# Kernel optimization log

Hardware: AMD Instinct MI355X
Metric: run time of the kernel (lower is better)

## Reference

```python
import jax, jax.numpy as jnp
import numpy as np

REGION_DIM = 144
LLM_DIM = 3584
NUM_HEADS = 4
HEAD_DIM = REGION_DIM // NUM_HEADS          # 36
V_HEAD_DIM = LLM_DIM // NUM_HEADS           # 896
LN_EPS = 1e-5
N, M = 4096, 4096


def setup_inputs() -> dict:
    key = jax.random.key(0)
    ks = jax.random.split(key, 16)
    s = 0.02
    return {
        "target_emb": jax.random.normal(ks[0], (N, REGION_DIM), jnp.float32),
        "source_emb": jax.random.normal(ks[1], (M, LLM_DIM), jnp.float32),
        "value_emb":  jax.random.normal(ks[2], (M, LLM_DIM), jnp.float32),
        # params stored [in, out] (transposed vs torch nn.Linear)
        "wq_w": jax.random.normal(ks[3], (REGION_DIM, REGION_DIM), jnp.float32) * s,
        "wq_b": jnp.zeros((REGION_DIM,), jnp.float32),
        "wk_w": jax.random.normal(ks[4], (LLM_DIM, REGION_DIM), jnp.float32) * s,
        "wk_b": jnp.zeros((REGION_DIM,), jnp.float32),
        # per-head V projections stacked: [H, llm_dim, llm_dim//H]
        "wv_w": jax.random.normal(ks[5], (NUM_HEADS, LLM_DIM, V_HEAD_DIM), jnp.float32) * s,
        "wv_b": jnp.zeros((NUM_HEADS, V_HEAD_DIM), jnp.float32),
        "resid_w": jax.random.normal(ks[6], (REGION_DIM, LLM_DIM), jnp.float32) * s,
        "resid_b": jnp.zeros((LLM_DIM,), jnp.float32),
        "out_w": jax.random.normal(ks[7], (LLM_DIM, LLM_DIM), jnp.float32) * s,
        "out_b": jnp.zeros((LLM_DIM,), jnp.float32),
        "ln_g": jnp.ones((LLM_DIM,), jnp.float32),
        "ln_b": jnp.zeros((LLM_DIM,), jnp.float32),
    }


def reference(target_emb, source_emb, value_emb,
              wq_w, wq_b, wk_w, wk_b, wv_w, wv_b,
              resid_w, resid_b, out_w, out_b, ln_g, ln_b):
    n = target_emb.shape[0]
    # Q: [N, region_dim] -> [H, N, head_dim]; K: [M, llm_dim] -> [H, M, head_dim]
    Q = (target_emb @ wq_w + wq_b).reshape(n, NUM_HEADS, HEAD_DIM).transpose(1, 0, 2)
    K = (source_emb @ wk_w + wk_b).reshape(-1, NUM_HEADS, HEAD_DIM).transpose(1, 0, 2)
    scores = jnp.einsum('hnd,hmd->hnm', Q, K) / jnp.sqrt(jnp.float32(HEAD_DIM))
    attn = jax.nn.softmax(scores, axis=-1)      # dropout = identity (eval mode)
    # per-head value projections: [H, M, llm_dim//H]
    V = jnp.einsum('me,hed->hmd', value_emb, wv_w) + wv_b[:, None, :]
    ctx = jnp.einsum('hnm,hmd->nhd', attn, V).reshape(n, LLM_DIM)
    x = ctx + (target_emb @ resid_w + resid_b)   # residual_proj (region_dim != llm_dim)
    mu = jnp.mean(x, axis=-1, keepdims=True)
    var = jnp.mean(jnp.square(x - mu), axis=-1, keepdims=True)
    x = (x - mu) * jax.lax.rsqrt(var + LN_EPS) * ln_g + ln_b
    return x @ out_w + out_b
```

## Files before the change

### kernel.cpp

```cpp
#include <hip/hip_runtime.h>

typedef _Float16 f16;
typedef _Float16 f16x8 __attribute__((ext_vector_type(8)));
typedef float f32x4 __attribute__((ext_vector_type(4)));

#define REGION_DIM 144
#define LLM_DIM 3584
#define NUM_HEADS 4
#define HEAD_DIM 36
#define HEAD_PAD 64
#define QK_COLS 256
#define KPAD_REGION 160
#define V_HEAD 896
#define LN_EPS 1e-5f

__device__ __forceinline__ void gl_lds16(const f16* g, f16* l)
{
    __builtin_amdgcn_global_load_lds(
        (const __attribute__((address_space(1))) unsigned int*)g,
        (__attribute__((address_space(3))) unsigned int*)l, 16, 0, 0);
}

#define S_BARRIER() do { asm volatile("" ::: "memory"); __builtin_amdgcn_s_barrier(); asm volatile("" ::: "memory"); } while (0)
#define WAIT_LGKM0() asm volatile("s_waitcnt lgkmcnt(0)" ::: "memory")
#define SCHED_FENCE() __builtin_amdgcn_sched_barrier(0)

__global__ void k_convert_pad(const float* __restrict__ in, f16* __restrict__ out,
                              int Cin, int Cout)
{
    int r = blockIdx.y;
    int c = blockIdx.x * 256 + threadIdx.x;
    if (c >= Cout) return;
    float v = (c < Cin) ? in[(long)r * Cin + c] : 0.f;
    out[(long)r * Cout + c] = (f16)v;
}

__global__ void k_transpose(const float* __restrict__ in, f16* __restrict__ out,
                            int R, int C, int Rpad, int Cpad,
                            long in_bstride, long out_bstride)
{
    __shared__ float tile[32][33];
    const float* ip = in + (long)blockIdx.z * in_bstride;
    f16* op = out + (long)blockIdx.z * out_bstride;
    int r0 = blockIdx.y * 32, c0 = blockIdx.x * 32;
    int tx = threadIdx.x, ty = threadIdx.y;
#pragma unroll
    for (int i = 0; i < 32; i += 8) {
        int r = r0 + ty + i, c = c0 + tx;
        tile[ty + i][tx] = (r < R && c < C) ? ip[(long)r * C + c] : 0.f;
    }
    __syncthreads();
#pragma unroll
    for (int i = 0; i < 32; i += 8) {
        int c = c0 + ty + i, r = r0 + tx;
        if (c < Cpad && r < Rpad) op[(long)c * Rpad + r] = (f16)tile[tx][ty + i];
    }
}

__global__ void k_headpad_w(const float* __restrict__ w, const float* __restrict__ b,
                            f16* __restrict__ outW, float* __restrict__ outB,
                            int E, int Epad)
{
    int hp = blockIdx.y;
    int h = hp >> 6, kk = hp & 63;
    int d = h * HEAD_DIM + kk;
    bool valid = (kk < HEAD_DIM);
    int e = blockIdx.x * 256 + threadIdx.x;
    if (e < Epad) {
        float v = (valid && e < E) ? w[(long)e * REGION_DIM + d] : 0.f;
        outW[(long)hp * Epad + e] = (f16)v;
    }
    if (blockIdx.x == 0 && threadIdx.x == 0) outB[hp] = valid ? b[d] : 0.f;
}

enum { EPI_F16_EXPSCALE = 0,
       EPI_F16_BIASROW  = 1,
       EPI_F16_DIVROW   = 2,
       EPI_F32_BIASCOL  = 3,
       EPI_F16_BIASCOL  = 4 };

template <int EPI>
__global__ __launch_bounds__(256, 2)
void gemm_f16(const f16* __restrict__ A, int lda, long sAz,
              const f16* __restrict__ Bt, int ldb, long sBz,
              void* __restrict__ Cv, int ldc, long sCz,
              const float* __restrict__ bias, long sbz, float scale, int K)
{
    __shared__ __align__(16) f16 sA[128 * 32];
    __shared__ __align__(16) f16 sB[128 * 32];
    const int tid = threadIdx.x;
    const int z = blockIdx.z;
    A += (long)z * sAz;
    Bt += (long)z * sBz;
    if (bias) bias += (long)z * sbz;

    const int gx = gridDim.x, gy = gridDim.y;
    int pid = blockIdx.y * gx + blockIdx.x;
    const int GROUP = 8;
    int span = GROUP * gx;
    int gid = pid / span;
    int y0 = gid * GROUP;
    int gsz = (gy - y0 < GROUP) ? (gy - y0) : GROUP;
    int rem = pid - gid * span;
    const int by = y0 + rem % gsz;
    const int bx = rem / gsz;
    const int m0 = by * 128, n0 = bx * 128;

    const int w = tid >> 6, l = tid & 63;
    const int wu = __builtin_amdgcn_readfirstlane(w);
    const int wr = w >> 1, wc = w & 1;

    f32x4 acc[4][4] = {};

    const int srow = tid >> 2;
    const int scol = (tid & 3) * 8;
    const f16* Ag = A + (long)(m0 + srow) * lda + scol;
    const f16* Bg = Bt + (long)(n0 + srow) * ldb + scol;
    f16* sA0 = sA + wu * 512;
    f16* sA1 = sA + 2048 + wu * 512;
    f16* sB0 = sB + wu * 512;
    f16* sB1 = sB + 2048 + wu * 512;
    const int qk = (l >> 4) * 8;
    const int fr = l & 15;

    for (int k0 = 0; k0 < K; k0 += 32) {
        __syncthreads();
        gl_lds16(Ag + k0, sA0);
        gl_lds16(Ag + (long)64 * lda + k0, sA1);
        gl_lds16(Bg + k0, sB0);
        gl_lds16(Bg + (long)64 * ldb + k0, sB1);
        __syncthreads();

        f16x8 af[4], bf[4];
#pragma unroll
        for (int mt = 0; mt < 4; mt++)
            af[mt] = *(const f16x8*)&sA[(wr * 64 + mt * 16 + fr) * 32 + qk];
#pragma unroll
        for (int nt = 0; nt < 4; nt++)
            bf[nt] = *(const f16x8*)&sB[(wc * 64 + nt * 16 + fr) * 32 + qk];
#pragma unroll
        for (int mt = 0; mt < 4; mt++)
#pragma unroll
            for (int nt = 0; nt < 4; nt++)
                acc[mt][nt] = __builtin_amdgcn_mfma_f32_16x16x32_f16(af[mt], bf[nt], acc[mt][nt], 0, 0, 0);
    }

    const int q4 = (l >> 4) * 4;
    float bc[4];
#pragma unroll
    for (int nt = 0; nt < 4; nt++) {
        if constexpr (EPI == EPI_F16_BIASCOL || EPI == EPI_F32_BIASCOL)
            bc[nt] = bias[n0 + wc * 64 + nt * 16 + fr];
        else
            bc[nt] = 0.f;
    }
#pragma unroll
    for (int mt = 0; mt < 4; mt++)
#pragma unroll
        for (int r = 0; r < 4; r++) {
            int row = m0 + wr * 64 + mt * 16 + q4 + r;
            float rowv = 0.f;
            if constexpr (EPI == EPI_F16_BIASROW) rowv = bias[row];
            if constexpr (EPI == EPI_F16_DIVROW) rowv = 1.f / bias[row];
#pragma unroll
            for (int nt = 0; nt < 4; nt++) {
                int col = n0 + wc * 64 + nt * 16 + fr;
                float v = acc[mt][nt][r];
                if constexpr (EPI == EPI_F16_EXPSCALE) {
                    ((f16*)Cv + (long)z * sCz)[(long)row * ldc + col] = (f16)__expf(v * scale);
                } else if constexpr (EPI == EPI_F16_BIASROW) {
                    ((f16*)Cv + (long)z * sCz)[(long)row * ldc + col] = (f16)(v + rowv);
                } else if constexpr (EPI == EPI_F16_DIVROW) {
                    ((f16*)Cv + (long)z * sCz)[(long)row * ldc + col] = (f16)(v * rowv);
                } else if constexpr (EPI == EPI_F16_BIASCOL) {
                    ((f16*)Cv + (long)z * sCz)[(long)row * ldc + col] = (f16)(v + bc[nt]);
                } else {
                    ((float*)Cv + (long)z * sCz)[(long)row * ldc + col] = v + bc[nt];
                }
            }
        }
}

template <int EPI>
__global__ __launch_bounds__(512, 2)
void gemm256_f16(const f16* __restrict__ A, int lda,
                 const f16* __restrict__ Bt, int ldb,
                 void* __restrict__ Cv, int ldc,
                 const float* __restrict__ bias, int K)
{
    __shared__ __align__(16) f16 sm[65536];
    f16* smf = sm;

    const int tid = threadIdx.x;
    const int l = tid & 63;

    const int gx = gridDim.x, gy = gridDim.y;
    int pid = blockIdx.y * gx + blockIdx.x;
    int nwg = gx * gy;
    int q = nwg >> 3, r8 = nwg & 7;
    int xcd = pid & 7, idx = pid >> 3;
    int swz = (xcd < r8) ? (xcd * (q + 1) + idx)
                         : (r8 * (q + 1) + (xcd - r8) * q + idx);
    const int by = swz % gy, bx = swz / gy;
    const int m0 = by * 256, n0 = bx * 256;

    const int wu = __builtin_amdgcn_readfirstlane(tid >> 6);
    const int wr = wu >> 2;
    const int wc = wu & 3;
    const int wst = wu * 512;

    const int strow = wu * 8 + (l >> 3);
    const int stcol = ((l & 7) ^ (l >> 3)) * 8;
    const f16* Asrc = A + (size_t)(m0 + strow) * lda + stcol;
    const f16* Bsrc = Bt + (size_t)(n0 + strow) * ldb + stcol;

    const int fr = l & 15;
    const int hi8 = (l >> 4) * 8;
    const int swl = (fr & 7) * 8;
    const int ca0 = hi8 ^ swl;
    const int ca1 = (32 + hi8) ^ swl;

    const int NT = K >> 6;

    f32x4 acc[8][4] = {};
    f16x8 af[4][2], bf0[2][2], bf1[2][2];

    gl_lds16(Asrc, smf + wst);
    gl_lds16(Asrc + (size_t)64 * lda, smf + 4096 + wst);
    gl_lds16(Bsrc, smf + 16384 + wst);
    gl_lds16(Bsrc + (size_t)64 * ldb, smf + 16384 + 4096 + wst);
    gl_lds16(Asrc + (size_t)128 * lda, smf + 8192 + wst);
    gl_lds16(Asrc + (size_t)192 * lda, smf + 8192 + 4096 + wst);
    gl_lds16(Bsrc + (size_t)128 * ldb, smf + 16384 + 8192 + wst);
    gl_lds16(Bsrc + (size_t)192 * ldb, smf + 16384 + 8192 + 4096 + wst);
    if (NT > 1) {
        gl_lds16(Bsrc + 64, smf + 32768 + 16384 + wst);
        gl_lds16(Bsrc + 64 + (size_t)64 * ldb, smf + 32768 + 16384 + 4096 + wst);
        gl_lds16(Asrc + 64, smf + 32768 + wst);
        gl_lds16(Asrc + 64 + (size_t)64 * lda, smf + 32768 + 4096 + wst);
        asm volatile("s_waitcnt vmcnt(4)" ::: "memory");
    } else {
        asm volatile("s_waitcnt vmcnt(0)" ::: "memory");
    }
    S_BARRIER();

#define MFMA16(MB, NB, BF)                                                            \
    _Pragma("unroll") for (int i = 0; i < 4; i++)                                     \
    _Pragma("unroll") for (int j = 0; j < 2; j++) {                                   \
        acc[MB + i][NB + j] = __builtin_amdgcn_mfma_f32_16x16x32_f16(                 \
            af[i][0], BF[j][0], acc[MB + i][NB + j], 0, 0, 0);                        \
        acc[MB + i][NB + j] = __builtin_amdgcn_mfma_f32_16x16x32_f16(                 \
            af[i][1], BF[j][1], acc[MB + i][NB + j], 0, 0, 0);                        \
    }

    for (int t = 0; t < NT; ++t) {
        const int p = t & 1;
        const f16* sAp = smf + (p << 15) + wr * 8192 + fr * 64;
        const f16* sBp = smf + (p << 15) + 16384 + wc * 4096 + fr * 64;

#pragma unroll
        for (int i = 0; i < 4; i++) {
            af[i][0] = *(const f16x8*)(sAp + i * 1024 + ca0);
            af[i][1] = *(const f16x8*)(sAp + i * 1024 + ca1);
        }
#pragma unroll
        for (int j = 0; j < 2; j++) {
            bf0[j][0] = *(const f16x8*)(sBp + j * 1024 + ca0);
            bf0[j][1] = *(const f16x8*)(sBp + j * 1024 + ca1);
        }
        if (t + 1 < NT) {
            const f16* s = Asrc + (size_t)128 * lda + (size_t)(t + 1) * 64;
            f16* d = smf + ((p ^ 1) << 15) + 8192 + wst;
            gl_lds16(s, d);
            gl_lds16(s + (size_t)64 * lda, d + 4096);
        }
        S_BARRIER();
        WAIT_LGKM0();
        SCHED_FENCE();
        __builtin_amdgcn_s_setprio(1);
        MFMA16(0, 0, bf0);
        __builtin_amdgcn_s_setprio(0);
        WAIT_LGKM0();
        S_BARRIER();

#pragma unroll
        for (int j = 0; j < 2; j++) {
            bf1[j][0] = *(const f16x8*)(sBp + 2048 + j * 1024 + ca0);
            bf1[j][1] = *(const f16x8*)(sBp + 2048 + j * 1024 + ca1);
        }
        if (t + 1 < NT) {
            const f16* s = Bsrc + (size_t)128 * ldb + (size_t)(t + 1) * 64;
            f16* d = smf + ((p ^ 1) << 15) + 16384 + 8192 + wst;
            gl_lds16(s, d);
            gl_lds16(s + (size_t)64 * ldb, d + 4096);
        }
        S_BARRIER();
        WAIT_LGKM0();
        SCHED_FENCE();
        __builtin_amdgcn_s_setprio(1);
        MFMA16(0, 2, bf1);
        __builtin_amdgcn_s_setprio(0);
        WAIT_LGKM0();
        S_BARRIER();

#pragma unroll
        for (int i = 0; i < 4; i++) {
            af[i][0] = *(const f16x8*)(sAp + 4096 + i * 1024 + ca0);
            af[i][1] = *(const f16x8*)(sAp + 4096 + i * 1024 + ca1);
        }
        if (t + 2 < NT) {
            const f16* s = Bsrc + (size_t)(t + 2) * 64;
            f16* d = smf + (p << 15) + 16384 + wst;
            gl_lds16(s, d);
            gl_lds16(s + (size_t)64 * ldb, d + 4096);
        }
        S_BARRIER();
        WAIT_LGKM0();
        SCHED_FENCE();
        __builtin_amdgcn_s_setprio(1);
        MFMA16(4, 2, bf1);
        __builtin_amdgcn_s_setprio(0);
        WAIT_LGKM0();
        S_BARRIER();

        if (t + 2 < NT) {
            const f16* s = Asrc + (size_t)(t + 2) * 64;
            f16* d = smf + (p << 15) + wst;
            gl_lds16(s, d);
            gl_lds16(s + (size_t)64 * lda, d + 4096);
        }
        S_BARRIER();
        __builtin_amdgcn_s_setprio(1);
        MFMA16(4, 0, bf0);
        __builtin_amdgcn_s_setprio(0);
        if (t + 2 < NT) {
            asm volatile("s_waitcnt vmcnt(4)" ::: "memory");
        } else if (t + 1 < NT) {
            asm volatile("s_waitcnt vmcnt(0)" ::: "memory");
        }
        S_BARRIER();
    }
#undef MFMA16

    const int q4 = (l >> 4) * 4;
    float bc[4];
#pragma unroll
    for (int nt = 0; nt < 4; nt++) {
        if constexpr (EPI == EPI_F16_BIASCOL || EPI == EPI_F32_BIASCOL)
            bc[nt] = bias[n0 + wc * 64 + nt * 16 + fr];
        else
            bc[nt] = 0.f;
    }
#pragma unroll
    for (int mt = 0; mt < 8; mt++)
#pragma unroll
        for (int r = 0; r < 4; r++) {
            int row = m0 + wr * 128 + mt * 16 + q4 + r;
            float rowv = 0.f;
            if constexpr (EPI == EPI_F16_BIASROW) rowv = bias[row];
            if constexpr (EPI == EPI_F16_DIVROW) rowv = 1.f / bias[row];
#pragma unroll
            for (int nt = 0; nt < 4; nt++) {
                int col = n0 + wc * 64 + nt * 16 + fr;
                float v = acc[mt][nt][r];
                if constexpr (EPI == EPI_F16_BIASROW) {
                    ((f16*)Cv)[(size_t)row * ldc + col] = (f16)(v + rowv);
                } else if constexpr (EPI == EPI_F16_DIVROW) {
                    ((f16*)Cv)[(size_t)row * ldc + col] = (f16)(v * rowv);
                } else if constexpr (EPI == EPI_F16_BIASCOL) {
                    ((f16*)Cv)[(size_t)row * ldc + col] = (f16)(v + bc[nt]);
                } else {
                    ((float*)Cv)[(size_t)row * ldc + col] = v + bc[nt];
                }
            }
        }
}

__global__ void k_rowsum(const f16* __restrict__ P, float* __restrict__ lsum,
                         long hstride)
{
    const f16x8* p8 = (const f16x8*)(P + (long)blockIdx.y * hstride + (long)blockIdx.x * 4096);
    int t = threadIdx.x, w = t >> 6, l = t & 63;
    f16x8 a = p8[t], b = p8[256 + t];
    float s = 0.f;
#pragma unroll
    for (int j = 0; j < 8; j++) s += (float)a[j] + (float)b[j];
#pragma unroll
    for (int o = 32; o; o >>= 1) s += __shfl_xor(s, o);
    __shared__ float red[4];
    if (l == 0) red[w] = s;
    __syncthreads();
    if (t == 0)
        lsum[(long)blockIdx.y * gridDim.x + blockIdx.x] = red[0] + red[1] + red[2] + red[3];
}

__global__ void k_layernorm(const f16* __restrict__ ctxp, const f16* __restrict__ resp,
                            const float* __restrict__ g, const float* __restrict__ be,
                            f16* __restrict__ out)
{
    long base = (long)blockIdx.x * LLM_DIM;
    const f16x8* c8 = (const f16x8*)(ctxp + base);
    const f16x8* r8 = (const f16x8*)(resp + base);
    int t = threadIdx.x, w = t >> 6, l = t & 63;
    bool has2 = t < 192;
    f16x8 a0 = c8[t], b0 = r8[t];
    f16x8 a1 = {}, b1 = {};
    if (has2) { a1 = c8[256 + t]; b1 = r8[256 + t]; }
    float v[16];
    float s = 0.f;
#pragma unroll
    for (int j = 0; j < 8; j++) { v[j] = (float)a0[j] + (float)b0[j]; s += v[j]; }
#pragma unroll
    for (int j = 0; j < 8; j++) v[8 + j] = (float)a1[j] + (float)b1[j];
    if (has2)
#pragma unroll
        for (int j = 0; j < 8; j++) s += v[8 + j];
#pragma unroll
    for (int o = 32; o; o >>= 1) s += __shfl_xor(s, o);
    __shared__ float r1[4];
    if (l == 0) r1[w] = s;
    __syncthreads();
    float mu = (r1[0] + r1[1] + r1[2] + r1[3]) * (1.f / LLM_DIM);
    float s2 = 0.f;
#pragma unroll
    for (int j = 0; j < 8; j++) { float d = v[j] - mu; s2 += d * d; }
    if (has2)
#pragma unroll
        for (int j = 8; j < 16; j++) { float d = v[j] - mu; s2 += d * d; }
#pragma unroll
    for (int o = 32; o; o >>= 1) s2 += __shfl_xor(s2, o);
    __shared__ float r2[4];
    if (l == 0) r2[w] = s2;
    __syncthreads();
    float var = (r2[0] + r2[1] + r2[2] + r2[3]) * (1.f / LLM_DIM);
    float inv = rsqrtf(var + LN_EPS);
    f16* op = out + base;
    f16x8 o0, o1;
#pragma unroll
    for (int j = 0; j < 8; j++) {
        int c = t * 8 + j;
        o0[j] = (f16)((v[j] - mu) * inv * g[c] + be[c]);
    }
    ((f16x8*)op)[t] = o0;
    if (has2) {
#pragma unroll
        for (int j = 0; j < 8; j++) {
            int c = (256 + t) * 8 + j;
            o1[j] = (f16)((v[8 + j] - mu) * inv * g[c] + be[c]);
        }
        ((f16x8*)op)[256 + t] = o1;
    }
}

extern "C" void kernel_launch(void* const* d_in, const int* in_sizes, int n_in,
                              void* d_out, int out_size, void* d_ws, size_t ws_size,
                              hipStream_t stream)
{
    const float* target  = (const float*)d_in[0];
    const float* source  = (const float*)d_in[1];
    const float* value   = (const float*)d_in[2];
    const float* wq_w    = (const float*)d_in[3];
    const float* wq_b    = (const float*)d_in[4];
    const float* wk_w    = (const float*)d_in[5];
    const float* wk_b    = (const float*)d_in[6];
    const float* wv_w    = (const float*)d_in[7];
    const float* wv_b    = (const float*)d_in[8];
    const float* resid_w = (const float*)d_in[9];
    const float* resid_b = (const float*)d_in[10];
    const float* out_w   = (const float*)d_in[11];
    const float* out_b   = (const float*)d_in[12];
    const float* ln_g    = (const float*)d_in[13];
    const float* ln_b    = (const float*)d_in[14];

    const int N = in_sizes[0] / REGION_DIM;
    const int M = in_sizes[1] / LLM_DIM;

    char* ws = (char*)d_ws;
    size_t off = 0;
    auto alloc = [&](size_t bytes) { void* p = ws + off; off += (bytes + 255) & ~(size_t)255; return p; };
    f16*   tgt16   = (f16*)alloc((size_t)N * KPAD_REGION * 2);
    f16*   residT  = (f16*)alloc((size_t)LLM_DIM * KPAD_REGION * 2);
    f16*   outT    = (f16*)alloc((size_t)LLM_DIM * LLM_DIM * 2);
    f16*   wqT     = (f16*)alloc((size_t)QK_COLS * KPAD_REGION * 2);
    float* biasK   = (float*)alloc(QK_COLS * 4);
    float* biasQ   = (float*)alloc(QK_COLS * 4);
    f16*   Qtmp    = (f16*)alloc((size_t)N * QK_COLS * 2);
    f16*   Ktmp    = (f16*)alloc((size_t)M * QK_COLS * 2);
    f16*   Vt      = (f16*)alloc((size_t)LLM_DIM * M * 2);
    f16*   residbf = (f16*)alloc((size_t)N * LLM_DIM * 2);
    f16*   ctx     = (f16*)alloc((size_t)N * LLM_DIM * 2);
    f16*   xln     = (f16*)alloc((size_t)N * LLM_DIM * 2);
    float* lsum    = (float*)alloc((size_t)2 * N * 4);
    const int HB = 2;
    char* U = (char*)alloc((size_t)HB * N * M * 2);
    f16* val16 = (f16*)U;
    f16* wvT   = (f16*)(U + (size_t)M * LLM_DIM * 2);
    f16* src16 = (f16*)U;
    f16* wkT   = (f16*)(U + (size_t)M * LLM_DIM * 2);
    f16* attnB = (f16*)U;
    (void)n_in; (void)out_size; (void)ws_size;

    dim3 tb(32, 8);

    k_convert_pad<<<dim3(1, N), 256, 0, stream>>>(target, tgt16, REGION_DIM, KPAD_REGION);
    k_transpose<<<dim3(LLM_DIM / 32, KPAD_REGION / 32, 1), tb, 0, stream>>>(
        resid_w, residT, REGION_DIM, LLM_DIM, KPAD_REGION, LLM_DIM, 0, 0);
    k_transpose<<<dim3(LLM_DIM / 32, LLM_DIM / 32, 1), tb, 0, stream>>>(
        out_w, outT, LLM_DIM, LLM_DIM, LLM_DIM, LLM_DIM, 0, 0);
    k_headpad_w<<<dim3(1, QK_COLS), 256, 0, stream>>>(wq_w, wq_b, wqT, biasQ, REGION_DIM, KPAD_REGION);

    gemm_f16<EPI_F16_BIASCOL><<<dim3(QK_COLS / 128, N / 128), 256, 0, stream>>>(
        tgt16, KPAD_REGION, 0, wqT, KPAD_REGION, 0, Qtmp, QK_COLS, 0, biasQ, 0, 1.f, KPAD_REGION);
    gemm_f16<EPI_F16_BIASCOL><<<dim3(LLM_DIM / 128, N / 128), 256, 0, stream>>>(
        tgt16, KPAD_REGION, 0, residT, KPAD_REGION, 0, residbf, LLM_DIM, 0, resid_b, 0, 1.f, KPAD_REGION);

    k_convert_pad<<<dim3(LLM_DIM / 256, M), 256, 0, stream>>>(value, val16, LLM_DIM, LLM_DIM);
    k_transpose<<<dim3(V_HEAD / 32, LLM_DIM / 32, NUM_HEADS), tb, 0, stream>>>(
        wv_w, wvT, LLM_DIM, V_HEAD, LLM_DIM, V_HEAD, (long)LLM_DIM * V_HEAD, (long)V_HEAD * LLM_DIM);
    gemm256_f16<EPI_F16_BIASROW><<<dim3(M / 256, LLM_DIM / 256), 512, 0, stream>>>(
        wvT, LLM_DIM, val16, LLM_DIM, Vt, M, wv_b, LLM_DIM);

    k_convert_pad<<<dim3(LLM_DIM / 256, M), 256, 0, stream>>>(source, src16, LLM_DIM, LLM_DIM);
    k_headpad_w<<<dim3(LLM_DIM / 256, QK_COLS), 256, 0, stream>>>(wk_w, wk_b, wkT, biasK, LLM_DIM, LLM_DIM);
    gemm_f16<EPI_F16_BIASCOL><<<dim3(QK_COLS / 128, M / 128), 256, 0, stream>>>(
        src16, LLM_DIM, 0, wkT, LLM_DIM, 0, Ktmp, QK_COLS, 0, biasK, 0, 1.f, LLM_DIM);

    const float sc = 0.16666667f;
    for (int h0 = 0; h0 < NUM_HEADS; h0 += HB) {
        gemm_f16<EPI_F16_EXPSCALE><<<dim3(M / 128, N / 128, HB), 256, 0, stream>>>(
            Qtmp + h0 * HEAD_PAD, QK_COLS, HEAD_PAD,
            Ktmp + h0 * HEAD_PAD, QK_COLS, HEAD_PAD,
            attnB, M, (long)N * M, nullptr, 0, sc, HEAD_PAD);
        k_rowsum<<<dim3(N, HB), 256, 0, stream>>>(attnB, lsum, (long)N * M);
        gemm_f16<EPI_F16_DIVROW><<<dim3(V_HEAD / 128, N / 128, HB), 256, 0, stream>>>(
            attnB, M, (long)N * M,
            Vt + (size_t)h0 * V_HEAD * M, M, (long)V_HEAD * M,
            ctx + (size_t)h0 * V_HEAD, LLM_DIM, V_HEAD, lsum, N, 1.f, M);
    }

    k_layernorm<<<N, 256, 0, stream>>>(ctx, residbf, ln_g, ln_b, xln);
    gemm256_f16<EPI_F32_BIASCOL><<<dim3(LLM_DIM / 256, N / 256), 512, 0, stream>>>(
        xln, LLM_DIM, outT, LLM_DIM, (float*)d_out, LLM_DIM, out_b, LLM_DIM);
}
```

Baseline: 845.6 us.

## Restructure GEMM main loop with double-buffered A fragments and fewer barriers

Reworks the GEMM K-loop schedule so A fragments are held in two register sets (af0/af1), and the next tile's first A fragment is prefetched from LDS at the end of the current iteration. Barriers drop from about eight per iteration to two or three, and full lgkmcnt(0) waits become partial lgkmcnt(4)/(8) waits. The global-to-LDS loads for the next half-tile of A and B are issued together. The aim is to overlap LDS reads with MFMA work and cut synchronization stalls, at the cost of more registers and a fragile hand-tuned wait-count ordering that could race or lower occupancy.

```diff
diff --git a/kernel.cpp b/kernel.cpp
--- a/kernel.cpp
+++ b/kernel.cpp
@@ -22,7 +22,6 @@
 }
 
 #define S_BARRIER() do { asm volatile("" ::: "memory"); __builtin_amdgcn_s_barrier(); asm volatile("" ::: "memory"); } while (0)
-#define WAIT_LGKM0() asm volatile("s_waitcnt lgkmcnt(0)" ::: "memory")
 #define SCHED_FENCE() __builtin_amdgcn_sched_barrier(0)
 
 __global__ void k_convert_pad(const float* __restrict__ in, f16* __restrict__ out,
@@ -223,14 +222,14 @@
     const int NT = K >> 6;
 
     f32x4 acc[8][4] = {};
-    f16x8 af[4][2], bf0[2][2], bf1[2][2];
+    f16x8 af0[4][2], af1[4][2], bf0[2][2], bf1[2][2];
 
     gl_lds16(Asrc, smf + wst);
     gl_lds16(Asrc + (size_t)64 * lda, smf + 4096 + wst);
+    gl_lds16(Asrc + (size_t)128 * lda, smf + 8192 + wst);
+    gl_lds16(Asrc + (size_t)192 * lda, smf + 8192 + 4096 + wst);
     gl_lds16(Bsrc, smf + 16384 + wst);
     gl_lds16(Bsrc + (size_t)64 * ldb, smf + 16384 + 4096 + wst);
-    gl_lds16(Asrc + (size_t)128 * lda, smf + 8192 + wst);
-    gl_lds16(Asrc + (size_t)192 * lda, smf + 8192 + 4096 + wst);
     gl_lds16(Bsrc + (size_t)128 * ldb, smf + 16384 + 8192 + wst);
     gl_lds16(Bsrc + (size_t)192 * ldb, smf + 16384 + 8192 + 4096 + wst);
     if (NT > 1) {
@@ -243,104 +242,104 @@
         asm volatile("s_waitcnt vmcnt(0)" ::: "memory");
     }
     S_BARRIER();
-
-#define MFMA16(MB, NB, BF)                                                            \
+    {
+        const f16* sAp0 = smf + wr * 8192 + fr * 64;
+#pragma unroll
+        for (int i = 0; i < 4; i++) {
+            af0[i][0] = *(const f16x8*)(sAp0 + i * 1024 + ca0);
+            af0[i][1] = *(const f16x8*)(sAp0 + i * 1024 + ca1);
+        }
+    }
+
+#define MFMA_Q(MB, NB, AF, BF)                                                        \
     _Pragma("unroll") for (int i = 0; i < 4; i++)                                     \
     _Pragma("unroll") for (int j = 0; j < 2; j++) {                                   \
         acc[MB + i][NB + j] = __builtin_amdgcn_mfma_f32_16x16x32_f16(                 \
-            af[i][0], BF[j][0], acc[MB + i][NB + j], 0, 0, 0);                        \
+            AF[i][0], BF[j][0], acc[MB + i][NB + j], 0, 0, 0);                        \
         acc[MB + i][NB + j] = __builtin_amdgcn_mfma_f32_16x16x32_f16(                 \
-            af[i][1], BF[j][1], acc[MB + i][NB + j], 0, 0, 0);                        \
+            AF[i][1], BF[j][1], acc[MB + i][NB + j], 0, 0, 0);                        \
     }
 
     for (int t = 0; t < NT; ++t) {
         const int p = t & 1;
         const f16* sAp = smf + (p << 15) + wr * 8192 + fr * 64;
         const f16* sBp = smf + (p << 15) + 16384 + wc * 4096 + fr * 64;
-
-#pragma unroll
-        for (int i = 0; i < 4; i++) {
-            af[i][0] = *(const f16x8*)(sAp + i * 1024 + ca0);
-            af[i][1] = *(const f16x8*)(sAp + i * 1024 + ca1);
-        }
+        const bool s1 = (t + 1 < NT), s2 = (t + 2 < NT);
+
 #pragma unroll
         for (int j = 0; j < 2; j++) {
             bf0[j][0] = *(const f16x8*)(sBp + j * 1024 + ca0);
             bf0[j][1] = *(const f16x8*)(sBp + j * 1024 + ca1);
         }
-        if (t + 1 < NT) {
-            const f16* s = Asrc + (size_t)128 * lda + (size_t)(t + 1) * 64;
-            f16* d = smf + ((p ^ 1) << 15) + 8192 + wst;
-            gl_lds16(s, d);
-            gl_lds16(s + (size_t)64 * lda, d + 4096);
-        }
-        S_BARRIER();
-        WAIT_LGKM0();
-        SCHED_FENCE();
-        __builtin_amdgcn_s_setprio(1);
-        MFMA16(0, 0, bf0);
-        __builtin_amdgcn_s_setprio(0);
-        WAIT_LGKM0();
-        S_BARRIER();
-
 #pragma unroll
         for (int j = 0; j < 2; j++) {
             bf1[j][0] = *(const f16x8*)(sBp + 2048 + j * 1024 + ca0);
             bf1[j][1] = *(const f16x8*)(sBp + 2048 + j * 1024 + ca1);
         }
-        if (t + 1 < NT) {
-            const f16* s = Bsrc + (size_t)128 * ldb + (size_t)(t + 1) * 64;
-            f16* d = smf + ((p ^ 1) << 15) + 16384 + 8192 + wst;
-            gl_lds16(s, d);
-            gl_lds16(s + (size_t)64 * ldb, d + 4096);
-        }
-        S_BARRIER();
-        WAIT_LGKM0();
+        if (s1) {
+            const f16* sa = Asrc + (size_t)128 * lda + (size_t)(t + 1) * 64;
+            f16* da = smf + ((p ^ 1) << 15) + 8192 + wst;
+            gl_lds16(sa, da);
+            gl_lds16(sa + (size_t)64 * lda, da + 4096);
+            const f16* sb = Bsrc + (size_t)128 * ldb + (size_t)(t + 1) * 64;
+            f16* db = smf + ((p ^ 1) << 15) + 16384 + 8192 + wst;
+            gl_lds16(sb, db);
+            gl_lds16(sb + (size_t)64 * ldb, db + 4096);
+        }
+        asm volatile("s_waitcnt lgkmcnt(4)" ::: "memory");
         SCHED_FENCE();
         __builtin_amdgcn_s_setprio(1);
-        MFMA16(0, 2, bf1);
+        MFMA_Q(0, 0, af0, bf0);
         __builtin_amdgcn_s_setprio(0);
-        WAIT_LGKM0();
-        S_BARRIER();
 
 #pragma unroll
         for (int i = 0; i < 4; i++) {
-            af[i][0] = *(const f16x8*)(sAp + 4096 + i * 1024 + ca0);
-            af[i][1] = *(const f16x8*)(sAp + 4096 + i * 1024 + ca1);
-        }
-        if (t + 2 < NT) {
-            const f16* s = Bsrc + (size_t)(t + 2) * 64;
-            f16* d = smf + (p << 15) + 16384 + wst;
-            gl_lds16(s, d);
-            gl_lds16(s + (size_t)64 * ldb, d + 4096);
-        }
-        S_BARRIER();
-        WAIT_LGKM0();
+            af1[i][0] = *(const f16x8*)(sAp + 4096 + i * 1024 + ca0);
+            af1[i][1] = *(const f16x8*)(sAp + 4096 + i * 1024 + ca1);
+        }
+        asm volatile("s_waitcnt lgkmcnt(8)" ::: "memory");
         SCHED_FENCE();
         __builtin_amdgcn_s_setprio(1);
-        MFMA16(4, 2, bf1);
+        MFMA_Q(0, 2, af0, bf1);
         __builtin_amdgcn_s_setprio(0);
-        WAIT_LGKM0();
+
         S_BARRIER();
-
-        if (t + 2 < NT) {
-            const f16* s = Asrc + (size_t)(t + 2) * 64;
-            f16* d = smf + (p << 15) + wst;
-            gl_lds16(s, d);
-            gl_lds16(s + (size_t)64 * lda, d + 4096);
-        }
+        if (s2) {
+            const f16* sb = Bsrc + (size_t)(t + 2) * 64;
+            f16* db = smf + (p << 15) + 16384 + wst;
+            gl_lds16(sb, db);
+            gl_lds16(sb + (size_t)64 * ldb, db + 4096);
+        }
+        asm volatile("s_waitcnt lgkmcnt(0)" ::: "memory");
+        SCHED_FENCE();
+        __builtin_amdgcn_s_setprio(1);
+        MFMA_Q(4, 2, af1, bf1);
+        __builtin_amdgcn_s_setprio(0);
+
         S_BARRIER();
+        if (s2) {
+            const f16* sa = Asrc + (size_t)(t + 2) * 64;
+            f16* da = smf + (p << 15) + wst;
+            gl_lds16(sa, da);
+            gl_lds16(sa + (size_t)64 * lda, da + 4096);
+            asm volatile("s_waitcnt vmcnt(4)" ::: "memory");
+        } else if (s1) {
+            asm volatile("s_waitcnt vmcnt(0)" ::: "memory");
+        }
+        if (s1) {
+            S_BARRIER();
+            const f16* sApN = smf + ((p ^ 1) << 15) + wr * 8192 + fr * 64;
+#pragma unroll
+            for (int i = 0; i < 4; i++) {
+                af0[i][0] = *(const f16x8*)(sApN + i * 1024 + ca0);
+                af0[i][1] = *(const f16x8*)(sApN + i * 1024 + ca1);
+            }
+        }
         __builtin_amdgcn_s_setprio(1);
-        MFMA16(4, 0, bf0);
+        MFMA_Q(4, 0, af1, bf0);
         __builtin_amdgcn_s_setprio(0);
-        if (t + 2 < NT) {
-            asm volatile("s_waitcnt vmcnt(4)" ::: "memory");
-        } else if (t + 1 < NT) {
-            asm volatile("s_waitcnt vmcnt(0)" ::: "memory");
-        }
-        S_BARRIER();
-    }
-#undef MFMA16
+    }
+#undef MFMA_Q
 
     const int q4 = (l >> 4) * 4;
     float bc[4];
```

New measurement: 845.5 us. About the same (-0.0%).
